# Kernel optimization log

Measured on AMD Instinct MI355X. Metric: run time of the kernel, lower is better.

The kernel has to match this reference:

```python
import jax, jax.numpy as jnp
import numpy as np

N = 100000   # nodes
E = 800000   # edges
H = 128      # hidden_dim
HOP = 3
B = 64       # graphs


def setup_inputs() -> dict:
    key = jax.random.key(0)
    ks = jax.random.split(key, 24)
    s = 0.05
    x = jnp.round(jax.random.uniform(ks[0], (N, 1))).astype(jnp.float32)  # binary node indicator
    edge_index = jax.random.randint(ks[1], (2, E), 0, N)
    edge_attr = jax.random.normal(ks[2], (E, 1), dtype=jnp.float32)
    batch = jnp.sort(jax.random.randint(ks[3], (N,), 0, B))
    p = lambda k, sh: (s * jax.random.normal(k, sh)).astype(jnp.float32)
    return dict(
        x=x, edge_index=edge_index, edge_attr=edge_attr, batch=batch, num_graphs=B,
        l0_w=p(ks[4], (HOP, 1, H)), l0_b=p(ks[5], (HOP, H)),
        l1_w=p(ks[6], (HOP, H, H)), l1_b=p(ks[7], (HOP, H)),
        l2_w=p(ks[8], (HOP, 1, H)), l2_b=p(ks[9], (HOP, H)),
        l3_w=p(ks[10], (HOP, 1, 1)), l3_b=p(ks[11], (HOP, 1)),
        att_w=p(ks[12], (2 * H, H)), att_b=p(ks[13], (H,)),
        sp_w=p(ks[14], (H, H)), sp_b=p(ks[15], (H,)),
        ac_w=p(ks[16], (2 * H, H)), ac_b=p(ks[17], (H,)),
        last_w=p(ks[18], (2 * H, 1)), last_b=p(ks[19], (1,)),
    )


def _seg_mean(v, idx, m):
    # scatter-mean into m buckets; empty buckets -> 0 (matches PyG MeanAggregation)
    s = jax.ops.segment_sum(v, idx, num_segments=m)
    c = jax.ops.segment_sum(jnp.ones((v.shape[0], 1), v.dtype), idx, num_segments=m)
    return jnp.where(c > 0, s / jnp.maximum(c, 1.0), 0.0)


def reference(x, edge_index, edge_attr, batch, num_graphs,
              l0_w, l0_b, l1_w, l1_b, l2_w, l2_b, l3_w, l3_b,
              att_w, att_b, sp_w, sp_b, ac_w, ac_b, last_w, last_b):
    n = x.shape[0]
    row, col = edge_index[0], edge_index[1]
    hop, hid = l0_w.shape[0], l0_w.shape[2]
    u = jnp.zeros((n, hid), x.dtype)
    for i in range(hop):
        first = x @ l0_w[i] + l0_b[i]                      # [N,H]
        u_agg = _seg_mean(edge_attr * u[col], row, n)      # gather + scatter-mean
        second = u_agg @ l1_w[i] + l1_b[i]
        ee = jax.nn.relu(edge_attr @ l3_w[i] + l3_b[i])    # [E,1]
        third = _seg_mean(ee, row, n) @ l2_w[i] + l2_b[i]
        u = jax.nn.relu(first + second + third)
    # per-graph cluster embeddings (global_mean_pool ratios)
    h_c_0 = _seg_mean(u * (1 - x), batch, num_graphs) / _seg_mean(1 - x, batch, num_graphs)
    h_c_1 = _seg_mean(u * x, batch, num_graphs) / _seg_mean(x, batch, num_graphs)
    hc0, hc1 = h_c_0[batch], h_c_1[batch]                  # [N,H]
    tce = x * hc0 + (1 - x) * hc1
    h_a = jnp.concatenate([u, tce], axis=-1)               # [N,2H]
    att = h_a @ att_w + att_b
    w0 = jnp.sum(att * hc0, axis=1, keepdims=True)
    w1 = jnp.sum(att * hc1, axis=1, keepdims=True)
    w = jax.nn.softmax(jnp.concatenate([w0, w1], axis=-1), axis=-1)
    h_s = w[:, :1] * hc0 + w[:, 1:] * hc1
    q = jnp.concatenate([h_s @ sp_w + sp_b, h_a @ ac_w + ac_b], axis=-1) @ last_w + last_b
    return q
```

## Files before the change

kernel.cpp:

```cpp
#include <hip/hip_runtime.h>
#include <stdint.h>

typedef unsigned int  u32;
typedef unsigned short u16;

typedef short bf16x8 __attribute__((ext_vector_type(8)));
typedef float f32x4  __attribute__((ext_vector_type(4)));

static __device__ __forceinline__ float b2f(u16 h){
    union { u32 u; float f; } v; v.u = ((u32)h) << 16; return v.f;
}
static __device__ __forceinline__ float b2f_hi(u32 w){
    union { u32 u; float f; } v; v.u = w & 0xFFFF0000u; return v.f;
}
static __device__ __forceinline__ float b2f_lo(u32 w){
    union { u32 u; float f; } v; v.u = w << 16; return v.f;
}
static __device__ __forceinline__ u16 f2b(float f){
    union { float f; u32 u; } v; v.f = f;
    u32 r = v.u + 0x7FFFu + ((v.u >> 16) & 1u);
    return (u16)(r >> 16);
}

#define OL0W 0
#define OL0B 384
#define OL1W 768
#define OL1B 49920
#define OL2W 50304
#define OL2B 50688
#define OL3W 51072
#define OL3B 51075
#define OATTW 51078
#define OATTB 83846
#define OSPW 83974
#define OSPB 100358
#define OACW 100486
#define OACB 133254
#define OLASTW 133382
#define OLASTB 133638
#define WTOT 133639

#define PREPW_BLOCKS 192
#define ECAP 40

struct Ptrs16 { const void* p[16]; };

static __device__ __forceinline__ int detect_bf(const u32* __restrict__ xw){
    int lane = threadIdx.x & 63;
    int f = 0;
    #pragma unroll
    for (int i = 0; i < 8; ++i){
        u32 w = xw[lane * 8 + i];
        f |= ((w & 0xFFFFu) == 0x3F80u) ? 1 : 0;
    }
    return __ballot(f) != 0ull;
}

__global__ __launch_bounds__(256) void k_prep(Ptrs16 wp, const void* __restrict__ xin,
                                              float* __restrict__ wc, float* __restrict__ xc,
                                              u16* __restrict__ w1t, float* __restrict__ basev,
                                              int* __restrict__ flag,
                                              const int* __restrict__ row, const int* __restrict__ col,
                                              const void* __restrict__ ea,
                                              int* __restrict__ cnt, int2* __restrict__ ecs,
                                              int scatBase, int E, int N){
    int b = blockIdx.x, t = threadIdx.x;
    int bf = detect_bf((const u32*)xin);
    if (b >= scatBase){
        int e0 = ((b - scatBase) * 256 + t) * 4;
        if (e0 >= E) return;
        int rr[4], cc[4]; float av[4];
        if (e0 + 3 < E){
            int4 rv = *(const int4*)(row + e0);
            int4 cv = *(const int4*)(col + e0);
            rr[0]=rv.x; rr[1]=rv.y; rr[2]=rv.z; rr[3]=rv.w;
            cc[0]=cv.x; cc[1]=cv.y; cc[2]=cv.z; cc[3]=cv.w;
            if (bf){
                ushort4 ev = *(const ushort4*)((const u16*)ea + e0);
                av[0]=b2f(ev.x); av[1]=b2f(ev.y); av[2]=b2f(ev.z); av[3]=b2f(ev.w);
            } else {
                float4 ev = *(const float4*)((const float*)ea + e0);
                av[0]=ev.x; av[1]=ev.y; av[2]=ev.z; av[3]=ev.w;
            }
        } else {
            #pragma unroll
            for (int j = 0; j < 4; ++j){
                int e = e0 + j;
                rr[j] = (e < E) ? row[e] : 0;
                cc[j] = (e < E) ? col[e] : 0;
                av[j] = (e < E) ? (bf ? b2f(((const u16*)ea)[e]) : ((const float*)ea)[e]) : 0.f;
            }
        }
        int slot[4];
        #pragma unroll
        for (int j = 0; j < 4; ++j)
            slot[j] = (e0 + j < E) ? atomicAdd(&cnt[rr[j]], 1) : ECAP;
        #pragma unroll
        for (int j = 0; j < 4; ++j)
            if (e0 + j < E && slot[j] < ECAP)
                ecs[(size_t)rr[j] * ECAP + slot[j]] = make_int2(cc[j], __float_as_int(av[j]));
        return;
    }
    auto rd = [&](int seg, int off) -> float {
        return bf ? b2f(((const u16*)wp.p[seg])[off]) : ((const float*)wp.p[seg])[off];
    };
    if (b < PREPW_BLOCKS){
        int id = b * 256 + t;
        int i = id >> 14, rem = id & 16383;
        int n = rem >> 7, k = rem & 127;
        w1t[(i * 128 + n) * 128 + k] = f2b(rd(2, (i * 128 + k) * 128 + n));
        if (id < 384) basev[id] = rd(1, id) + rd(3, id) + rd(5, id);
        if (id == 0) *flag = bf;
    } else {
        int i = (b - PREPW_BLOCKS) * 256 + t;
        const int sz[16] = {384,384,49152,384,384,384,3,3,32768,128,16384,128,32768,128,256,1};
        if (i < WTOT){
            int seg = 0, off = i;
            while (off >= sz[seg]){ off -= sz[seg]; ++seg; }
            wc[i] = rd(seg, off);
        } else {
            int n = i - WTOT;
            if (n < N) xc[n] = bf ? b2f(((const u16*)xin)[n]) : ((const float*)xin)[n];
        }
    }
}

__global__ __launch_bounds__(256) void k_hop0(const int2* __restrict__ ecs, const int* __restrict__ cnt,
                                              const float* __restrict__ xc, const float* __restrict__ wc,
                                              float* __restrict__ t12, const float* __restrict__ basev,
                                              float* __restrict__ spf, float* __restrict__ acf,
                                              float* __restrict__ biasv,
                                              uint4* __restrict__ uOut, int foldBlk, int N){
    if ((int)blockIdx.x == foldBlk){
        int t = threadIdx.x;
        const float* aw  = wc + OACW + t * 128;
        const float* lw2 = wc + OLASTW + 128;
        float s = 0.f;
        #pragma unroll 8
        for (int o = 0; o < 128; ++o) s += aw[o] * lw2[o];
        acf[t] = s;
        if (t < 128){
            const float* sw = wc + OSPW + t * 128;
            const float* lw = wc + OLASTW;
            float s2 = 0.f;
            #pragma unroll 8
            for (int o = 0; o < 128; ++o) s2 += sw[o] * lw[o];
            spf[t] = s2;
        }
        float pb = 0.f;
        if (t < 128) pb = wc[OSPB + t] * wc[OLASTW + t] + wc[OACB + t] * wc[OLASTW + 128 + t];
        __shared__ float red[4];
        #pragma unroll
        for (int m = 1; m < 64; m <<= 1) pb += __shfl_xor(pb, m);
        if ((t & 63) == 0) red[t >> 6] = pb;
        __syncthreads();
        if (t == 0) biasv[0] = red[0] + red[1] + red[2] + red[3] + wc[OLASTB];
        return;
    }
    int id = blockIdx.x * 256 + threadIdx.x;
    int n = id >> 4;
    if (n >= N) return;
    int sl = threadIdx.x & 15;
    float w30 = wc[OL3W + 0], w31 = wc[OL3W + 1], w32 = wc[OL3W + 2];
    float c30 = wc[OL3B + 0], c31 = wc[OL3B + 1], c32 = wc[OL3B + 2];
    int d = min(cnt[n], ECAP);
    size_t s = (size_t)n * ECAP;
    float s0 = 0.f, s1 = 0.f, s2 = 0.f;
    for (int e = sl; e < d; e += 16){
        float a = __int_as_float(ecs[s + e].y);
        s0 += fmaxf(a * w30 + c30, 0.f);
        s1 += fmaxf(a * w31 + c31, 0.f);
        s2 += fmaxf(a * w32 + c32, 0.f);
    }
    #pragma unroll
    for (int m = 1; m < 16; m <<= 1){
        s0 += __shfl_xor(s0, m);
        s1 += __shfl_xor(s1, m);
        s2 += __shfl_xor(s2, m);
    }
    float iv = d > 0 ? 1.0f / (float)d : 0.f;
    if (sl == 0){ t12[n] = s1 * iv; t12[N + n] = s2 * iv; }
    float t0 = s0 * iv;
    float xv = xc[n];
    int j = sl * 8;
    const float* l0wc = wc + OL0W;
    const float* l2wc = wc + OL2W;
    u32 w[4];
    #pragma unroll
    for (int k = 0; k < 4; ++k){
        float va = fmaxf(xv * l0wc[j + 2*k]     + t0 * l2wc[j + 2*k]     + basev[j + 2*k],     0.f);
        float vb = fmaxf(xv * l0wc[j + 2*k + 1] + t0 * l2wc[j + 2*k + 1] + basev[j + 2*k + 1], 0.f);
        w[k] = (u32)f2b(va) | ((u32)f2b(vb) << 16);
    }
    uOut[id] = make_uint4(w[0], w[1], w[2], w[3]);
}

#define ACC8(acc, g, p) \
    acc[0] += g * b2f_lo(p.x); acc[1] += g * b2f_hi(p.x); \
    acc[2] += g * b2f_lo(p.y); acc[3] += g * b2f_hi(p.y); \
    acc[4] += g * b2f_lo(p.z); acc[5] += g * b2f_hi(p.z); \
    acc[6] += g * b2f_lo(p.w); acc[7] += g * b2f_hi(p.w);

template<int POOL>
__global__ __launch_bounds__(256) void k_hop(const u16* __restrict__ uPrev, u16* __restrict__ uNext,
    const int2* __restrict__ ecs, const int* __restrict__ cnt,
    const u16* __restrict__ w1t, const float* __restrict__ basev,
    const float* __restrict__ l0wc, const float* __restrict__ l2wc,
    const float* __restrict__ xc, const float* __restrict__ t_i,
    const int* __restrict__ batch, float* __restrict__ S0, float* __restrict__ S1,
    int* __restrict__ cnt1, int N)
{
    __shared__ __align__(16) u16 A[32][136];
    int tid = threadIdx.x;
    int lane = tid & 63, wid = tid >> 6;
    int n0 = blockIdx.x * 32;
    int cid = lane & 15, grp = lane >> 4;

    #pragma unroll
    for (int p = 0; p < 2; ++p){
        int r = wid * 8 + p * 4 + grp;
        int n = n0 + r;
        float acc[8];
        #pragma unroll
        for (int j = 0; j < 8; ++j) acc[j] = 0.f;
        if (n < N){
            int d = min(cnt[n], ECAP);
            size_t s = (size_t)n * ECAP;
            for (int e = 0; e < d; e += 4){
                int i1 = (e + 1 < d) ? e + 1 : 0;
                int i2 = (e + 2 < d) ? e + 2 : 0;
                int i3 = (e + 3 < d) ? e + 3 : 0;
                int2 m0 = ecs[s + e], m1 = ecs[s + i1], m2 = ecs[s + i2], m3 = ecs[s + i3];
                float g0 = __int_as_float(m0.y);
                float g1 = (e + 1 < d) ? __int_as_float(m1.y) : 0.f;
                float g2 = (e + 2 < d) ? __int_as_float(m2.y) : 0.f;
                float g3 = (e + 3 < d) ? __int_as_float(m3.y) : 0.f;
                uint4 p0 = *(const uint4*)(uPrev + (size_t)m0.x * 128 + cid * 8);
                uint4 p1 = *(const uint4*)(uPrev + (size_t)m1.x * 128 + cid * 8);
                uint4 p2 = *(const uint4*)(uPrev + (size_t)m2.x * 128 + cid * 8);
                uint4 p3 = *(const uint4*)(uPrev + (size_t)m3.x * 128 + cid * 8);
                ACC8(acc, g0, p0); ACC8(acc, g1, p1);
                ACC8(acc, g2, p2); ACC8(acc, g3, p3);
            }
            float sc = d > 0 ? 1.0f / (float)d : 0.f;
            uint4 o;
            o.x = (u32)f2b(acc[0] * sc) | ((u32)f2b(acc[1] * sc) << 16);
            o.y = (u32)f2b(acc[2] * sc) | ((u32)f2b(acc[3] * sc) << 16);
            o.z = (u32)f2b(acc[4] * sc) | ((u32)f2b(acc[5] * sc) << 16);
            o.w = (u32)f2b(acc[6] * sc) | ((u32)f2b(acc[7] * sc) << 16);
            *(uint4*)&A[r][cid * 8] = o;
        } else {
            *(uint4*)&A[r][cid * 8] = make_uint4(0u, 0u, 0u, 0u);
        }
    }
    __syncthreads();

    bf16x8 bfr[4][2];
    #pragma unroll
    for (int kk = 0; kk < 4; ++kk)
        #pragma unroll
        for (int nt = 0; nt < 2; ++nt)
            bfr[kk][nt] = *(const bf16x8*)(w1t + (size_t)(wid * 32 + nt * 16 + cid) * 128 + kk * 32 + grp * 8);

    f32x4 acc4[2][2];
    #pragma unroll
    for (int mt = 0; mt < 2; ++mt)
        #pragma unroll
        for (int nt = 0; nt < 2; ++nt) acc4[mt][nt] = (f32x4){0.f, 0.f, 0.f, 0.f};
    #pragma unroll
    for (int kk = 0; kk < 4; ++kk){
        int kb = kk * 32 + grp * 8;
        bf16x8 af[2];
        #pragma unroll
        for (int mt = 0; mt < 2; ++mt) af[mt] = *(const bf16x8*)&A[mt * 16 + cid][kb];
        #pragma unroll
        for (int mt = 0; mt < 2; ++mt)
            #pragma unroll
            for (int nt = 0; nt < 2; ++nt)
                acc4[mt][nt] = __builtin_amdgcn_mfma_f32_16x16x32_bf16(af[mt], bfr[kk][nt], acc4[mt][nt], 0, 0, 0);
    }

    float w0c[2], w2c[2], bc[2]; int colv[2];
    #pragma unroll
    for (int nt = 0; nt < 2; ++nt){
        int col = wid * 32 + nt * 16 + cid;
        colv[nt] = col;
        w0c[nt] = l0wc[col]; w2c[nt] = l2wc[col]; bc[nt] = basev[col];
    }
    int gLo = 0, gHi = 0;
    float accP[8];
    if (POOL){
        gLo = batch[n0];
        gHi = batch[min(n0 + 31, N - 1)];
        #pragma unroll
        for (int j = 0; j < 8; ++j) accP[j] = 0.f;
    }
    #pragma unroll
    for (int mt = 0; mt < 2; ++mt){
        #pragma unroll
        for (int rg = 0; rg < 4; ++rg){
            int n = n0 + mt * 16 + grp * 4 + rg;
            if (n < N){
                float xv = xc[n];
                float tv = t_i[n];
                int sel = 0;
                if (POOL){
                    sel = ((batch[n] != gLo) ? 2 : 0) + ((xv > 0.5f) ? 1 : 0);
                }
                #pragma unroll
                for (int nt = 0; nt < 2; ++nt){
                    float v = fmaxf(acc4[mt][nt][rg] + xv * w0c[nt] + tv * w2c[nt] + bc[nt], 0.f);
                    uNext[(size_t)n * 128 + colv[nt]] = f2b(v);
                    if (POOL) accP[nt * 4 + sel] += v;
                }
            }
        }
    }
    if (POOL){
        #pragma unroll
        for (int j = 0; j < 8; ++j){
            accP[j] += __shfl_xor(accP[j], 16);
            accP[j] += __shfl_xor(accP[j], 32);
        }
        if (grp == 0){
            #pragma unroll
            for (int nt = 0; nt < 2; ++nt){
                atomicAdd(&S0[gLo * 128 + colv[nt]], accP[nt * 4 + 0]);
                atomicAdd(&S1[gLo * 128 + colv[nt]], accP[nt * 4 + 1]);
                if (gHi != gLo){
                    atomicAdd(&S0[gHi * 128 + colv[nt]], accP[nt * 4 + 2]);
                    atomicAdd(&S1[gHi * 128 + colv[nt]], accP[nt * 4 + 3]);
                }
            }
        }
        if (wid == 0){
            int n = n0 + lane;
            int ok = (lane < 32 && n < N) ? 1 : 0;
            int is1 = ok && (xc[n] > 0.5f);
            int hi  = ok && (batch[n] != gLo);
            unsigned long long mLo = __ballot(is1 && !hi);
            unsigned long long mHi = __ballot(is1 && hi);
            if (lane == 0){
                int c = __popcll(mLo);
                if (c) atomicAdd(&cnt1[gLo], c);
                c = __popcll(mHi);
                if (c && gHi != gLo) atomicAdd(&cnt1[gHi], c);
            }
        }
    }
}


static __device__ __forceinline__ int lowbound(const int* b, int n, int g){
    int lo = 0, hi = n;
    while (lo < hi){ int m = (lo + hi) >> 1; if (b[m] < g) lo = m + 1; else hi = m; }
    return lo;
}

__global__ __launch_bounds__(256) void k_graph(const float* __restrict__ S0, const float* __restrict__ S1,
                                               const int* __restrict__ cnt1, const int* __restrict__ batch,
                                               const float* __restrict__ wc, const float* __restrict__ spf,
                                               const float* __restrict__ acf,
                                               float* __restrict__ v0, float* __restrict__ v1,
                                               float* __restrict__ gsc, int N){
    __shared__ float h0[128], h1[128], sv0[128], sv1[128];
    int g = blockIdx.x, t = threadIdx.x;
    int st = lowbound(batch, N, g), en = lowbound(batch, N, g + 1);
    int c1 = cnt1[g], c0 = (en - st) - c1;
    if (t < 128){
        h0[t] = c0 > 0 ? S0[g * 128 + t] / (float)c0 : 0.f;
        h1[t] = c1 > 0 ? S1[g * 128 + t] / (float)c1 : 0.f;
    }
    __syncthreads();
    float a0 = 0.f, a1 = 0.f;
    for (int o = 0; o < 128; ++o){
        float w = wc[OATTW + t * 128 + o];
        a0 += w * h0[o];
        a1 += w * h1[o];
    }
    v0[g * 256 + t] = a0; v1[g * 256 + t] = a1;
    if (t >= 128){ sv0[t - 128] = a0; sv1[t - 128] = a1; }
    __syncthreads();
    if (t < 64){
        int l = t;
        float p[10];
        #pragma unroll
        for (int k = 0; k < 10; ++k) p[k] = 0.f;
        #pragma unroll
        for (int rep = 0; rep < 2; ++rep){
            int o = l + rep * 64;
            float hh0 = h0[o], hh1 = h1[o];
            float q0 = sv0[o], q1 = sv1[o];
            float ab = wc[OATTB + o];
            float sf = spf[o], af = acf[128 + o];
            p[0] += q0 * hh0; p[1] += q0 * hh1;
            p[2] += q1 * hh0; p[3] += q1 * hh1;
            p[4] += ab * hh0; p[5] += ab * hh1;
            p[6] += sf * hh0; p[7] += sf * hh1;
            p[8] += af * hh0; p[9] += af * hh1;
        }
        #pragma unroll
        for (int m = 1; m < 64; m <<= 1){
            #pragma unroll
            for (int k = 0; k < 10; ++k) p[k] += __shfl_xor(p[k], m);
        }
        if (l == 0){
            #pragma unroll
            for (int k = 0; k < 10; ++k) gsc[g * 10 + k] = p[k];
        }
    }
}

__global__ __launch_bounds__(256) void k_final(const u16* __restrict__ u, const float* __restrict__ xc,
                                               const int* __restrict__ batch,
                                               const float* __restrict__ v0, const float* __restrict__ v1,
                                               const float* __restrict__ acf, const float* __restrict__ gsc,
                                               const float* __restrict__ biasv, const int* __restrict__ flag,
                                               void* __restrict__ out, int N){
    int bf = *flag;
    int lane = threadIdx.x & 63, wid = threadIdx.x >> 6;
    int sub = lane >> 4, cid = lane & 15;
    int n = blockIdx.x * 16 + wid * 4 + sub;
    if (n >= N) return;
    int g = batch[n];
    int ch = cid * 8;
    uint4 uv = *(const uint4*)(u + (size_t)n * 128 + ch);
    const float* pv0 = v0 + g * 256 + ch;
    const float* pv1 = v1 + g * 256 + ch;
    const float* pac = acf + ch;
    float uu[8] = {b2f_lo(uv.x), b2f_hi(uv.x), b2f_lo(uv.y), b2f_hi(uv.y),
                   b2f_lo(uv.z), b2f_hi(uv.z), b2f_lo(uv.w), b2f_hi(uv.w)};
    float r0 = 0.f, r1 = 0.f, rA = 0.f;
    #pragma unroll
    for (int j = 0; j < 8; ++j){ r0 += uu[j] * pv0[j]; r1 += uu[j] * pv1[j]; rA += uu[j] * pac[j]; }
    #pragma unroll
    for (int m = 1; m < 16; m <<= 1){
        r0 += __shfl_xor(r0, m);
        r1 += __shfl_xor(r1, m);
        rA += __shfl_xor(rA, m);
    }
    if (cid == 0){
        const float* G = gsc + g * 10;
        bool xv = xc[n] > 0.5f;
        float z0 = r0 + (xv ? G[0] : G[1]) + G[4];
        float z1 = r1 + (xv ? G[2] : G[3]) + G[5];
        float mz = fmaxf(z0, z1);
        float e0 = expf(z0 - mz), e1 = expf(z1 - mz);
        float inv = 1.f / (e0 + e1);
        float q = (e0 * G[6] + e1 * G[7]) * inv + rA + (xv ? G[8] : G[9]) + biasv[0];
        if (bf) ((u16*)out)[n] = f2b(q);
        else    ((float*)out)[n] = q;
    }
}


extern "C" void kernel_launch(void* const* d_in, const int* in_sizes, int n_in,
                              void* d_out, int out_size, void* d_ws, size_t ws_size,
                              hipStream_t stream)
{
    const void* x    = d_in[0];
    const int* ei    = (const int*)d_in[1];
    const void* ea   = d_in[2];
    const int* batch = (const int*)d_in[3];
    Ptrs16 wp;
    for (int i = 0; i < 16; ++i) wp.p[i] = d_in[5 + i];

    int N = in_sizes[0];
    int E = in_sizes[2];
    const int* rowI = ei;
    const int* colI = ei + E;

    char* w = (char*)d_ws;
    size_t o = 0;
    auto alloc = [&](size_t b) -> char* {
        char* p = w + o; o = (o + b + 255) & ~(size_t)255; return p;
    };
    int*   flag   = (int*)alloc(4);
    float* basev  = (float*)alloc(3 * 128 * 4);
    float* spf    = (float*)alloc(128 * 4);
    float* acf    = (float*)alloc(256 * 4);
    float* biasv  = (float*)alloc(4);
    float* gsc    = (float*)alloc(64 * 10 * 4);
    float* v0     = (float*)alloc(64 * 256 * 4);
    float* v1     = (float*)alloc(64 * 256 * 4);
    float* wc     = (float*)alloc((size_t)WTOT * 4);
    float* xc     = (float*)alloc((size_t)N * 4);
    float* t12    = (float*)alloc((size_t)2 * N * 4);
    u16*   w1t    = (u16*)alloc((size_t)3 * 128 * 128 * 2);
    u16*   uA     = (u16*)alloc((size_t)N * 128 * 2);
    u16*   uB     = (u16*)alloc((size_t)N * 128 * 2);
    int2*  ecs    = (int2*)alloc((size_t)N * ECAP * 8);
    int*   cnt    = (int*)alloc((size_t)N * 4);
    float* S0     = (float*)alloc(64 * 128 * 4);
    float* S1     = (float*)alloc(64 * 128 * 4);
    int*   cnt1   = (int*)alloc(64 * 4);
    (void)ws_size; (void)n_in; (void)out_size;

    hipMemsetAsync(cnt, 0, (size_t)((char*)cnt1 - (char*)cnt) + 64 * 4, stream);

    int gE4 = (E / 4 + 255) / 256 + 1;
    int canonB = (WTOT + N + 255) / 256;
    int scatBase = PREPW_BLOCKS + canonB;

    k_prep<<<scatBase + gE4, 256, 0, stream>>>(wp, x, wc, xc, w1t, basev, flag,
                                               rowI, colI, ea, cnt, ecs, scatBase, E, N);
    int gHop0 = (N * 16 + 255) / 256;
    k_hop0<<<gHop0 + 1, 256, 0, stream>>>(ecs, cnt, xc, wc, t12, basev, spf, acf, biasv,
                                          (uint4*)uA, gHop0, N);

    int gHop = (N + 31) / 32;
    k_hop<0><<<gHop, 256, 0, stream>>>(uA, uB, ecs, cnt,
                                       w1t + 1 * 16384, basev + 128, wc + OL0W + 128, wc + OL2W + 128,
                                       xc, t12, batch, S0, S1, cnt1, N);
    k_hop<1><<<gHop, 256, 0, stream>>>(uB, uA, ecs, cnt,
                                       w1t + 2 * 16384, basev + 256, wc + OL0W + 256, wc + OL2W + 256,
                                       xc, t12 + N, batch, S0, S1, cnt1, N);

    k_graph<<<64, 256, 0, stream>>>(S0, S1, cnt1, batch, wc, spf, acf, v0, v1, gsc, N);
    k_final<<<(N + 15) / 16, 256, 0, stream>>>(uA, xc, batch, v0, v1, acf, gsc, biasv, flag, d_out, N);
}
```

Measured before the change: 304.3 us.

## Software-pipeline edge gathers across two rows and use packed bf16 convert

The per-node neighbour gather in the hop kernel is restructured. Each thread group now handles two rows at once, stages the first 16 edge descriptors in shared memory, and issues the next batch of four neighbour loads before consuming the current one, so more gathers are in flight. Edges beyond 16 fall back to a simple loop. Float-to-bf16 packing also switches to the hardware v_cvt_pk_bf16_f32 instruction, which adds register pressure and inline asm that depends on the target.

```diff
diff --git a/kernel.cpp b/kernel.cpp
--- a/kernel.cpp
+++ b/kernel.cpp
@@ -20,6 +20,14 @@
     union { float f; u32 u; } v; v.f = f;
     u32 r = v.u + 0x7FFFu + ((v.u >> 16) & 1u);
     return (u16)(r >> 16);
+}
+static __device__ __forceinline__ u32 cvt_pk(float lo, float hi){
+    u32 r; asm("v_cvt_pk_bf16_f32 %0, %1, %2" : "=v"(r) : "v"(lo), "v"(hi));
+    return r;
+}
+static __device__ __forceinline__ u16 f2b1(float f){
+    u32 r; asm("v_cvt_pk_bf16_f32 %0, %1, %2" : "=v"(r) : "v"(f), "v"(f));
+    return (u16)r;
 }
 
 #define OL0W 0
@@ -190,7 +198,7 @@
     for (int k = 0; k < 4; ++k){
         float va = fmaxf(xv * l0wc[j + 2*k]     + t0 * l2wc[j + 2*k]     + basev[j + 2*k],     0.f);
         float vb = fmaxf(xv * l0wc[j + 2*k + 1] + t0 * l2wc[j + 2*k + 1] + basev[j + 2*k + 1], 0.f);
-        w[k] = (u32)f2b(va) | ((u32)f2b(vb) << 16);
+        w[k] = cvt_pk(va, vb);
     }
     uOut[id] = make_uint4(w[0], w[1], w[2], w[3]);
 }
@@ -200,6 +208,20 @@
     acc[2] += g * b2f_lo(p.y); acc[3] += g * b2f_hi(p.y); \
     acc[4] += g * b2f_lo(p.z); acc[5] += g * b2f_hi(p.z); \
     acc[6] += g * b2f_lo(p.w); acc[7] += g * b2f_hi(p.w);
+
+#define ISSUE(r_, m_, b_, P_, G_) { \
+    _Pragma("unroll") \
+    for (int j_ = 0; j_ < 4; ++j_){ \
+        int e_ = (b_) * 4 + j_; \
+        int ok_ = e_ < (m_); \
+        int2 mm_ = esh[r_][ok_ ? e_ : 0]; \
+        G_[j_] = ok_ ? __int_as_float(mm_.y) : 0.f; \
+        P_[j_] = *(const uint4*)(uPrev + (size_t)mm_.x * 128 + coff); \
+    } }
+
+#define CONSUME(P_, G_, a_) { \
+    ACC8(a_, G_[0], P_[0]); ACC8(a_, G_[1], P_[1]); \
+    ACC8(a_, G_[2], P_[2]); ACC8(a_, G_[3], P_[3]); }
 
 template<int POOL>
 __global__ __launch_bounds__(256) void k_hop(const u16* __restrict__ uPrev, u16* __restrict__ uNext,
@@ -211,47 +233,81 @@
     int* __restrict__ cnt1, int N)
 {
     __shared__ __align__(16) u16 A[32][136];
+    __shared__ __align__(8) int2 esh[32][17];
     int tid = threadIdx.x;
     int lane = tid & 63, wid = tid >> 6;
     int n0 = blockIdx.x * 32;
     int cid = lane & 15, grp = lane >> 4;
-
-    #pragma unroll
-    for (int p = 0; p < 2; ++p){
-        int r = wid * 8 + p * 4 + grp;
-        int n = n0 + r;
-        float acc[8];
-        #pragma unroll
-        for (int j = 0; j < 8; ++j) acc[j] = 0.f;
-        if (n < N){
-            int d = min(cnt[n], ECAP);
-            size_t s = (size_t)n * ECAP;
-            for (int e = 0; e < d; e += 4){
-                int i1 = (e + 1 < d) ? e + 1 : 0;
-                int i2 = (e + 2 < d) ? e + 2 : 0;
-                int i3 = (e + 3 < d) ? e + 3 : 0;
-                int2 m0 = ecs[s + e], m1 = ecs[s + i1], m2 = ecs[s + i2], m3 = ecs[s + i3];
-                float g0 = __int_as_float(m0.y);
-                float g1 = (e + 1 < d) ? __int_as_float(m1.y) : 0.f;
-                float g2 = (e + 2 < d) ? __int_as_float(m2.y) : 0.f;
-                float g3 = (e + 3 < d) ? __int_as_float(m3.y) : 0.f;
-                uint4 p0 = *(const uint4*)(uPrev + (size_t)m0.x * 128 + cid * 8);
-                uint4 p1 = *(const uint4*)(uPrev + (size_t)m1.x * 128 + cid * 8);
-                uint4 p2 = *(const uint4*)(uPrev + (size_t)m2.x * 128 + cid * 8);
-                uint4 p3 = *(const uint4*)(uPrev + (size_t)m3.x * 128 + cid * 8);
-                ACC8(acc, g0, p0); ACC8(acc, g1, p1);
-                ACC8(acc, g2, p2); ACC8(acc, g3, p3);
-            }
-            float sc = d > 0 ? 1.0f / (float)d : 0.f;
-            uint4 o;
-            o.x = (u32)f2b(acc[0] * sc) | ((u32)f2b(acc[1] * sc) << 16);
-            o.y = (u32)f2b(acc[2] * sc) | ((u32)f2b(acc[3] * sc) << 16);
-            o.z = (u32)f2b(acc[4] * sc) | ((u32)f2b(acc[5] * sc) << 16);
-            o.w = (u32)f2b(acc[6] * sc) | ((u32)f2b(acc[7] * sc) << 16);
-            *(uint4*)&A[r][cid * 8] = o;
-        } else {
-            *(uint4*)&A[r][cid * 8] = make_uint4(0u, 0u, 0u, 0u);
-        }
+    int coff = cid * 8;
+
+    int rA = wid * 8 + grp;
+    int rB = rA + 4;
+    int nA = n0 + rA, nB = n0 + rB;
+
+    int dA = 0, dB = 0;
+    if (nA < N){ dA = min(cnt[nA], ECAP); esh[rA][cid] = ecs[(size_t)nA * ECAP + cid]; }
+    if (nB < N){ dB = min(cnt[nB], ECAP); esh[rB][cid] = ecs[(size_t)nB * ECAP + cid]; }
+    int mA = min(dA, 16), mB = min(dB, 16);
+    int nbA = (mA + 3) >> 2, nbB = (mB + 3) >> 2;
+
+    float aA[8], aB[8];
+    #pragma unroll
+    for (int j = 0; j < 8; ++j){ aA[j] = 0.f; aB[j] = 0.f; }
+
+    uint4 PA[4], PB[4]; float GA[4], GB[4];
+    if (nbA > 0) ISSUE(rA, mA, 0, PA, GA);
+    if (nbB > 0) ISSUE(rB, mB, 0, PB, GB);
+    int nbM = nbA > nbB ? nbA : nbB;
+    for (int b = 0; b < nbM; ++b){
+        if (b < nbA){
+            CONSUME(PA, GA, aA);
+            if (b + 1 < nbA) ISSUE(rA, mA, b + 1, PA, GA);
+        }
+        if (b < nbB){
+            CONSUME(PB, GB, aB);
+            if (b + 1 < nbB) ISSUE(rB, mB, b + 1, PB, GB);
+        }
+    }
+    if (dA > 16){
+        size_t s = (size_t)nA * ECAP;
+        for (int e = 16; e < dA; ++e){
+            int2 m = ecs[s + e];
+            float g = __int_as_float(m.y);
+            uint4 p = *(const uint4*)(uPrev + (size_t)m.x * 128 + coff);
+            ACC8(aA, g, p);
+        }
+    }
+    if (dB > 16){
+        size_t s = (size_t)nB * ECAP;
+        for (int e = 16; e < dB; ++e){
+            int2 m = ecs[s + e];
+            float g = __int_as_float(m.y);
+            uint4 p = *(const uint4*)(uPrev + (size_t)m.x * 128 + coff);
+            ACC8(aB, g, p);
+        }
+    }
+
+    if (nA < N){
+        float sc = dA > 0 ? 1.0f / (float)dA : 0.f;
+        uint4 o;
+        o.x = cvt_pk(aA[0] * sc, aA[1] * sc);
+        o.y = cvt_pk(aA[2] * sc, aA[3] * sc);
+        o.z = cvt_pk(aA[4] * sc, aA[5] * sc);
+        o.w = cvt_pk(aA[6] * sc, aA[7] * sc);
+        *(uint4*)&A[rA][coff] = o;
+    } else {
+        *(uint4*)&A[rA][coff] = make_uint4(0u, 0u, 0u, 0u);
+    }
+    if (nB < N){
+        float sc = dB > 0 ? 1.0f / (float)dB : 0.f;
+        uint4 o;
+        o.x = cvt_pk(aB[0] * sc, aB[1] * sc);
+        o.y = cvt_pk(aB[2] * sc, aB[3] * sc);
+        o.z = cvt_pk(aB[4] * sc, aB[5] * sc);
+        o.w = cvt_pk(aB[6] * sc, aB[7] * sc);
+        *(uint4*)&A[rB][coff] = o;
+    } else {
+        *(uint4*)&A[rB][coff] = make_uint4(0u, 0u, 0u, 0u);
     }
     __syncthreads();
 
@@ -310,7 +366,7 @@
                 #pragma unroll
                 for (int nt = 0; nt < 2; ++nt){
                     float v = fmaxf(acc4[mt][nt][rg] + xv * w0c[nt] + tv * w2c[nt] + bc[nt], 0.f);
-                    uNext[(size_t)n * 128 + colv[nt]] = f2b(v);
+                    uNext[(size_t)n * 128 + colv[nt]] = f2b1(v);
                     if (POOL) accP[nt * 4 + sel] += v;
                 }
             }
```

After: 312.0 us. 2.5% more time.

## Split hop into feature-sliced gather kernel and separate MFMA matmul kernel

Applied to the files above, without the earlier changes.

The fused gather+matmul hop kernel is split in two. A new k_gather kernel aggregates neighbor features over 8 column slices of 16 features each, reading a slice-major (transposed) copy of u so each slice's random gathers stay within a small, cache-resident region. k_mm then loads the aggregated rows and does the MFMA projection, writing u in the sliced layout when the next hop needs it. Nontemporal loads and stores plus a packed bf16 convert instruction are added throughout; the split costs an extra round trip of the aggregate buffer through memory and extra kernel launches.

```diff
diff --git a/kernel.cpp b/kernel.cpp
--- a/kernel.cpp
+++ b/kernel.cpp
@@ -6,6 +6,8 @@
 
 typedef short bf16x8 __attribute__((ext_vector_type(8)));
 typedef float f32x4  __attribute__((ext_vector_type(4)));
+typedef u32 u32x2v __attribute__((ext_vector_type(2)));
+typedef u32 u32x4v __attribute__((ext_vector_type(4)));
 
 static __device__ __forceinline__ float b2f(u16 h){
     union { u32 u; float f; } v; v.u = ((u32)h) << 16; return v.f;
@@ -20,6 +22,27 @@
     union { float f; u32 u; } v; v.f = f;
     u32 r = v.u + 0x7FFFu + ((v.u >> 16) & 1u);
     return (u16)(r >> 16);
+}
+static __device__ __forceinline__ u32 cvt_pk(float lo, float hi){
+    u32 r; asm("v_cvt_pk_bf16_f32 %0, %1, %2" : "=v"(r) : "v"(lo), "v"(hi));
+    return r;
+}
+static __device__ __forceinline__ u16 f2b1(float f){
+    u32 r; asm("v_cvt_pk_bf16_f32 %0, %1, %2" : "=v"(r) : "v"(f), "v"(f));
+    return (u16)r;
+}
+
+static __device__ __forceinline__ int2 nt_ld2(const int2* p){
+    u32x2v v = __builtin_nontemporal_load((const u32x2v*)p);
+    return make_int2((int)v[0], (int)v[1]);
+}
+static __device__ __forceinline__ uint4 nt_ld4(const u16* p){
+    u32x4v v = __builtin_nontemporal_load((const u32x4v*)p);
+    return make_uint4(v[0], v[1], v[2], v[3]);
+}
+static __device__ __forceinline__ void nt_st2(u16* p, u32 a, u32 b){
+    u32x2v v; v[0] = a; v[1] = b;
+    __builtin_nontemporal_store(v, (u32x2v*)p);
 }
 
 #define OL0W 0
@@ -42,6 +65,7 @@
 
 #define PREPW_BLOCKS 192
 #define ECAP 40
+#define NSLICE 8
 
 struct Ptrs16 { const void* p[16]; };
 
@@ -97,8 +121,10 @@
             slot[j] = (e0 + j < E) ? atomicAdd(&cnt[rr[j]], 1) : ECAP;
         #pragma unroll
         for (int j = 0; j < 4; ++j)
-            if (e0 + j < E && slot[j] < ECAP)
-                ecs[(size_t)rr[j] * ECAP + slot[j]] = make_int2(cc[j], __float_as_int(av[j]));
+            if (e0 + j < E && slot[j] < ECAP){
+                u32x2v v; v[0] = (u32)cc[j]; v[1] = (u32)__float_as_int(av[j]);
+                __builtin_nontemporal_store(v, (u32x2v*)&ecs[(size_t)rr[j] * ECAP + slot[j]]);
+            }
         return;
     }
     auto rd = [&](int seg, int off) -> float {
@@ -130,7 +156,7 @@
                                               float* __restrict__ t12, const float* __restrict__ basev,
                                               float* __restrict__ spf, float* __restrict__ acf,
                                               float* __restrict__ biasv,
-                                              uint4* __restrict__ uOut, int foldBlk, int N){
+                                              u16* __restrict__ uOut, int foldBlk, int N){
     if ((int)blockIdx.x == foldBlk){
         int t = threadIdx.x;
         const float* aw  = wc + OACW + t * 128;
@@ -190,20 +216,69 @@
     for (int k = 0; k < 4; ++k){
         float va = fmaxf(xv * l0wc[j + 2*k]     + t0 * l2wc[j + 2*k]     + basev[j + 2*k],     0.f);
         float vb = fmaxf(xv * l0wc[j + 2*k + 1] + t0 * l2wc[j + 2*k + 1] + basev[j + 2*k + 1], 0.f);
-        w[k] = (u32)f2b(va) | ((u32)f2b(vb) << 16);
-    }
-    uOut[id] = make_uint4(w[0], w[1], w[2], w[3]);
-}
-
-#define ACC8(acc, g, p) \
-    acc[0] += g * b2f_lo(p.x); acc[1] += g * b2f_hi(p.x); \
-    acc[2] += g * b2f_lo(p.y); acc[3] += g * b2f_hi(p.y); \
-    acc[4] += g * b2f_lo(p.z); acc[5] += g * b2f_hi(p.z); \
-    acc[6] += g * b2f_lo(p.w); acc[7] += g * b2f_hi(p.w);
-
-template<int POOL>
-__global__ __launch_bounds__(256) void k_hop(const u16* __restrict__ uPrev, u16* __restrict__ uNext,
-    const int2* __restrict__ ecs, const int* __restrict__ cnt,
+        w[k] = cvt_pk(va, vb);
+    }
+    *(uint4*)(uOut + ((size_t)(sl >> 1) * N + n) * 16 + (sl & 1) * 8) =
+        make_uint4(w[0], w[1], w[2], w[3]);
+}
+
+__global__ __launch_bounds__(256) void k_gather(const u16* __restrict__ uT, u16* __restrict__ agg,
+                                                const int2* __restrict__ ecs, const int* __restrict__ cnt,
+                                                int N){
+    __shared__ int2 esh[32][17];
+    int tid = threadIdx.x;
+    int s  = blockIdx.x & 7;
+    int nb = blockIdx.x >> 3;
+    int nl = tid >> 3, l = tid & 7;
+    int n  = nb * 32 + nl;
+    const u16* us = uT + (size_t)s * N * 16;
+    int d = 0;
+    if (n < N) d = min(cnt[n], ECAP);
+    size_t sb = (size_t)n * ECAP;
+    if (l < d)     esh[nl][l]     = nt_ld2(&ecs[sb + l]);
+    if (l + 8 < d) esh[nl][l + 8] = nt_ld2(&ecs[sb + l + 8]);
+    int m = min(d, 16);
+    int half = l >> 2, cl = l & 3;
+    float a0 = 0.f, a1 = 0.f, a2 = 0.f, a3 = 0.f;
+    if (m > 0){
+        int idx = half;
+        int ok = idx < m;
+        int2 mc = esh[nl][ok ? idx : 0];
+        float gc = ok ? __int_as_float(mc.y) : 0.f;
+        uint2 uc = *(const uint2*)(us + (size_t)mc.x * 16 + cl * 4);
+        for (int e = 2; e < m; e += 2){
+            int i2 = e + half;
+            int o2 = i2 < m;
+            int2 mn = esh[nl][o2 ? i2 : 0];
+            float gn = o2 ? __int_as_float(mn.y) : 0.f;
+            uint2 un = *(const uint2*)(us + (size_t)mn.x * 16 + cl * 4);
+            a0 += gc * b2f_lo(uc.x); a1 += gc * b2f_hi(uc.x);
+            a2 += gc * b2f_lo(uc.y); a3 += gc * b2f_hi(uc.y);
+            gc = gn; uc = un;
+        }
+        a0 += gc * b2f_lo(uc.x); a1 += gc * b2f_hi(uc.x);
+        a2 += gc * b2f_lo(uc.y); a3 += gc * b2f_hi(uc.y);
+        for (int e = 16; e < d; e += 2){
+            int i2 = e + half;
+            int o2 = i2 < d;
+            int2 mn = o2 ? ecs[sb + i2] : make_int2(0, 0);
+            float gn = o2 ? __int_as_float(mn.y) : 0.f;
+            uint2 un = *(const uint2*)(us + (size_t)mn.x * 16 + cl * 4);
+            a0 += gn * b2f_lo(un.x); a1 += gn * b2f_hi(un.x);
+            a2 += gn * b2f_lo(un.y); a3 += gn * b2f_hi(un.y);
+        }
+    }
+    a0 += __shfl_xor(a0, 4); a1 += __shfl_xor(a1, 4);
+    a2 += __shfl_xor(a2, 4); a3 += __shfl_xor(a3, 4);
+    if (n < N && half == 0){
+        float sc = d > 0 ? 1.0f / (float)d : 0.f;
+        nt_st2(agg + (size_t)n * 128 + s * 16 + cl * 4,
+               cvt_pk(a0 * sc, a1 * sc), cvt_pk(a2 * sc, a3 * sc));
+    }
+}
+
+template<int POOL, int OUTT>
+__global__ __launch_bounds__(256) void k_mm(const u16* __restrict__ agg, u16* __restrict__ uNext,
     const u16* __restrict__ w1t, const float* __restrict__ basev,
     const float* __restrict__ l0wc, const float* __restrict__ l2wc,
     const float* __restrict__ xc, const float* __restrict__ t_i,
@@ -217,41 +292,13 @@
     int cid = lane & 15, grp = lane >> 4;
 
     #pragma unroll
-    for (int p = 0; p < 2; ++p){
-        int r = wid * 8 + p * 4 + grp;
-        int n = n0 + r;
-        float acc[8];
-        #pragma unroll
-        for (int j = 0; j < 8; ++j) acc[j] = 0.f;
-        if (n < N){
-            int d = min(cnt[n], ECAP);
-            size_t s = (size_t)n * ECAP;
-            for (int e = 0; e < d; e += 4){
-                int i1 = (e + 1 < d) ? e + 1 : 0;
-                int i2 = (e + 2 < d) ? e + 2 : 0;
-                int i3 = (e + 3 < d) ? e + 3 : 0;
-                int2 m0 = ecs[s + e], m1 = ecs[s + i1], m2 = ecs[s + i2], m3 = ecs[s + i3];
-                float g0 = __int_as_float(m0.y);
-                float g1 = (e + 1 < d) ? __int_as_float(m1.y) : 0.f;
-                float g2 = (e + 2 < d) ? __int_as_float(m2.y) : 0.f;
-                float g3 = (e + 3 < d) ? __int_as_float(m3.y) : 0.f;
-                uint4 p0 = *(const uint4*)(uPrev + (size_t)m0.x * 128 + cid * 8);
-                uint4 p1 = *(const uint4*)(uPrev + (size_t)m1.x * 128 + cid * 8);
-                uint4 p2 = *(const uint4*)(uPrev + (size_t)m2.x * 128 + cid * 8);
-                uint4 p3 = *(const uint4*)(uPrev + (size_t)m3.x * 128 + cid * 8);
-                ACC8(acc, g0, p0); ACC8(acc, g1, p1);
-                ACC8(acc, g2, p2); ACC8(acc, g3, p3);
-            }
-            float sc = d > 0 ? 1.0f / (float)d : 0.f;
-            uint4 o;
-            o.x = (u32)f2b(acc[0] * sc) | ((u32)f2b(acc[1] * sc) << 16);
-            o.y = (u32)f2b(acc[2] * sc) | ((u32)f2b(acc[3] * sc) << 16);
-            o.z = (u32)f2b(acc[4] * sc) | ((u32)f2b(acc[5] * sc) << 16);
-            o.w = (u32)f2b(acc[6] * sc) | ((u32)f2b(acc[7] * sc) << 16);
-            *(uint4*)&A[r][cid * 8] = o;
-        } else {
-            *(uint4*)&A[r][cid * 8] = make_uint4(0u, 0u, 0u, 0u);
-        }
+    for (int i = 0; i < 2; ++i){
+        int idx = i * 256 + tid;
+        int row = idx >> 4, part = idx & 15;
+        int nn = n0 + row;
+        uint4 v = make_uint4(0u, 0u, 0u, 0u);
+        if (nn < N) v = nt_ld4(agg + (size_t)nn * 128 + part * 8);
+        *(uint4*)&A[row][part * 8] = v;
     }
     __syncthreads();
 
@@ -310,7 +357,11 @@
                 #pragma unroll
                 for (int nt = 0; nt < 2; ++nt){
                     float v = fmaxf(acc4[mt][nt][rg] + xv * w0c[nt] + tv * w2c[nt] + bc[nt], 0.f);
-                    uNext[(size_t)n * 128 + colv[nt]] = f2b(v);
+                    if (OUTT)
+                        __builtin_nontemporal_store(f2b1(v),
+                            &uNext[((size_t)(colv[nt] >> 4) * N + n) * 16 + (colv[nt] & 15)]);
+                    else
+                        __builtin_nontemporal_store(f2b1(v), &uNext[(size_t)n * 128 + colv[nt]]);
                     if (POOL) accP[nt * 4 + sel] += v;
                 }
             }
@@ -506,16 +557,19 @@
                                                rowI, colI, ea, cnt, ecs, scatBase, E, N);
     int gHop0 = (N * 16 + 255) / 256;
     k_hop0<<<gHop0 + 1, 256, 0, stream>>>(ecs, cnt, xc, wc, t12, basev, spf, acf, biasv,
-                                          (uint4*)uA, gHop0, N);
-
-    int gHop = (N + 31) / 32;
-    k_hop<0><<<gHop, 256, 0, stream>>>(uA, uB, ecs, cnt,
-                                       w1t + 1 * 16384, basev + 128, wc + OL0W + 128, wc + OL2W + 128,
-                                       xc, t12, batch, S0, S1, cnt1, N);
-    k_hop<1><<<gHop, 256, 0, stream>>>(uB, uA, ecs, cnt,
-                                       w1t + 2 * 16384, basev + 256, wc + OL0W + 256, wc + OL2W + 256,
-                                       xc, t12 + N, batch, S0, S1, cnt1, N);
+                                          uA, gHop0, N);
+
+    int gMM = (N + 31) / 32;
+    int gG  = gMM * NSLICE;
+    k_gather<<<gG, 256, 0, stream>>>(uA, uB, ecs, cnt, N);
+    k_mm<0, 1><<<gMM, 256, 0, stream>>>(uB, uA,
+                                        w1t + 1 * 16384, basev + 128, wc + OL0W + 128, wc + OL2W + 128,
+                                        xc, t12, batch, S0, S1, cnt1, N);
+    k_gather<<<gG, 256, 0, stream>>>(uA, uB, ecs, cnt, N);
+    k_mm<1, 0><<<gMM, 256, 0, stream>>>(uB, uB,
+                                        w1t + 2 * 16384, basev + 256, wc + OL0W + 256, wc + OL2W + 256,
+                                        xc, t12 + N, batch, S0, S1, cnt1, N);
 
     k_graph<<<64, 256, 0, stream>>>(S0, S1, cnt1, batch, wc, spf, acf, v0, v1, gsc, N);
-    k_final<<<(N + 15) / 16, 256, 0, stream>>>(uA, xc, batch, v0, v1, acf, gsc, biasv, flag, d_out, N);
-}
+    k_final<<<(N + 15) / 16, 256, 0, stream>>>(uB, xc, batch, v0, v1, acf, gsc, biasv, flag, d_out, N);
+}
```

Result: slower. 452.6 us (+48.8%).
